# Kernel tuning notes

Measured on AMD Instinct MI355X. Metric: run time of the kernel, lower is better.

Reference implementation:

```python
import jax, jax.numpy as jnp
import numpy as np

DECAY = 0.99
EPS = 1e-05
BETA = 0.25
N_CODES = 1024
CODE_DIM = 128


def setup_inputs() -> dict:
    key = jax.random.key(0)
    k1, k2, k3, k4 = jax.random.split(key, 4)
    z_e = jax.random.normal(k1, (32, CODE_DIM, 32, 32), dtype=jnp.float32)
    embed = jax.random.normal(k2, (N_CODES, CODE_DIM), dtype=jnp.float32)
    cluster_size = jax.random.uniform(k3, (N_CODES,), dtype=jnp.float32) * 10.0
    embed_avg = jax.random.normal(k4, (N_CODES, CODE_DIM), dtype=jnp.float32)
    return {"z_e": z_e, "embed": embed, "cluster_size": cluster_size, "embed_avg": embed_avg}


def reference(z_e, embed, cluster_size, embed_avg):
    B, C, H, W = z_e.shape
    n_codes = embed.shape[0]
    # (B,C,H,W) -> (B*H*W, C)
    flat = jnp.transpose(z_e, (0, 2, 3, 1)).reshape(-1, C).astype(jnp.float32)
    e = embed.astype(jnp.float32)
    d = (flat ** 2).sum(1, keepdims=True) - 2.0 * flat @ e.T + (e ** 2).sum(1)
    idx = jnp.argmin(d, axis=1)
    z_q = embed[idx].reshape(B, H, W, C)
    z_q = jnp.transpose(z_q, (0, 3, 1, 2))  # (B,C,H,W)

    # ---- EMA codebook update (training branch, no-grad in torch) ----
    counts = jax.ops.segment_sum(jnp.ones_like(idx, dtype=jnp.float32), idx,
                                 num_segments=n_codes)
    new_cluster_size = cluster_size * DECAY + (1.0 - DECAY) * counts
    embed_sum = jax.ops.segment_sum(flat, idx, num_segments=n_codes)  # == (flat.T @ one_hot).T
    new_embed_avg = embed_avg * DECAY + (1.0 - DECAY) * embed_sum
    n = new_cluster_size.sum()
    denom = n + n_codes * EPS
    cs = (new_cluster_size + EPS) / denom * n
    cs_safe = jnp.maximum(cs, EPS)[:, None]
    embed_normalized = new_embed_avg / cs_safe
    embed_normalized = jnp.nan_to_num(embed_normalized, nan=0.0, posinf=1.0, neginf=-1.0)
    new_embed = jnp.clip(embed_normalized, -2.0, 2.0)

    # straight-through estimator
    z_q_st = z_e + jax.lax.stop_gradient(z_q - z_e)
    diff = jax.lax.stop_gradient(z_q_st).astype(jnp.float32) - z_e.astype(jnp.float32)
    loss = BETA * jnp.mean(diff ** 2)

    return (z_q_st, loss, idx.reshape(B, H, W), z_q, z_e,
            new_embed, new_cluster_size, new_embed_avg)
```

## Files before the change

### kernel.cpp

```cpp
#include <hip/hip_runtime.h>

#define DECAY 0.99f
#define ONE_MINUS_DECAY 0.01f
#define EPSF 1e-5f
#define BETA 0.25f

constexpr int M_ = 32768;
constexpr int N_ = 1024;
constexpr int K_ = 128;

typedef _Float16 f16;
typedef f16 f16x8 __attribute__((ext_vector_type(8)));
typedef float f32x4 __attribute__((ext_vector_type(4)));

#define GLOAD_LDS(g, l) __builtin_amdgcn_global_load_lds( \
    (const __attribute__((address_space(1))) void*)(g),   \
    (__attribute__((address_space(3))) void*)(l), 16, 0, 0)

#define PINS(p) { unsigned _t2 = m1 > (p) ? m1 : (p); m1 = m1 < (p) ? m1 : (p); \
                  unsigned _t3 = m2 > _t2 ? m2 : _t2;  m2 = m2 < _t2 ? m2 : _t2; \
                  m3 = m3 < _t3 ? m3 : _t3; }

constexpr size_t WS_FLAT   = 0;
constexpr size_t WS_XH     = WS_FLAT   + (size_t)M_ * K_ * 4;
constexpr size_t WS_EH     = WS_XH     + (size_t)M_ * K_ * 2;
constexpr size_t WS_NL     = WS_EH     + (size_t)N_ * K_ * 2;
constexpr size_t WS_PPK    = WS_NL     + (size_t)N_ * 4;
constexpr size_t WS_IDX    = WS_PPK    + (size_t)4 * M_ * 16;
constexpr size_t WS_COUNTS = WS_IDX    + (size_t)M_ * 4;
constexpr size_t WS_CUR    = WS_COUNTS + (size_t)N_ * 4;
constexpr size_t WS_ESUM   = WS_CUR    + (size_t)N_ * 4;
constexpr size_t WS_OFFS   = WS_ESUM   + (size_t)N_ * K_ * 4;
constexpr size_t WS_ROWS   = WS_OFFS   + (size_t)N_ * 4;
constexpr size_t WS_LPART  = WS_ROWS   + (size_t)M_ * 4;
constexpr size_t WS_NSUM   = WS_LPART  + (size_t)4096 * 8;

constexpr size_t O_ZQST = 0;
constexpr size_t O_LOSS = O_ZQST + (size_t)M_ * K_;
constexpr size_t O_IDX  = O_LOSS + 1;
constexpr size_t O_ZQ   = O_IDX  + (size_t)M_;
constexpr size_t O_ZE   = O_ZQ   + (size_t)M_ * K_;
constexpr size_t O_EMB  = O_ZE   + (size_t)M_ * K_;
constexpr size_t O_NCS  = O_EMB  + (size_t)N_ * K_;
constexpr size_t O_NEA  = O_NCS  + (size_t)N_;

__global__ void transpose_kernel(const float* __restrict__ ze,
                                 const float* __restrict__ embed,
                                 float* __restrict__ flat,
                                 f16* __restrict__ xh,
                                 float* __restrict__ out_ze,
                                 f16* __restrict__ eh, float* __restrict__ nl,
                                 uint4* __restrict__ zero8k) {
    __shared__ float tile[128][33];
    __shared__ float ered[2];
    const int j = blockIdx.x;
    const int t = threadIdx.x;
    if (t < 128) {
        float a = embed[(size_t)j * K_ + t];
        eh[(size_t)j * K_ + t] = (f16)(-2.f * a);
        float s = a * a;
        #pragma unroll
        for (int off = 32; off; off >>= 1) s += __shfl_down(s, off);
        if ((t & 63) == 0) ered[t >> 6] = s;
    }
    if (j < 2) zero8k[j * 256 + t] = make_uint4(0u, 0u, 0u, 0u);

    int b = j >> 5, h = j & 31;
    const size_t base = (size_t)b * 131072 + (size_t)h * 32;
    #pragma unroll
    for (int i = 0; i < 4; ++i) {
        int q = i * 256 + t;
        int c = q >> 3, w4 = (q & 7) * 4;
        float4 v = *(const float4*)(ze + base + (size_t)c * 1024 + w4);
        tile[c][w4 + 0] = v.x; tile[c][w4 + 1] = v.y;
        tile[c][w4 + 2] = v.z; tile[c][w4 + 3] = v.w;
        *(float4*)(out_ze + base + (size_t)c * 1024 + w4) = v;
    }
    __syncthreads();
    if (t == 0) nl[j] = ered[0] + ered[1];
    const int r0 = b * 1024 + h * 32;
    #pragma unroll
    for (int i = 0; i < 2; ++i) {
        int w = (t >> 4) + i * 16;
        int c0 = (t & 15) * 8;
        int r = r0 + w;
        float vv[8];
        #pragma unroll
        for (int q = 0; q < 8; ++q) vv[q] = tile[c0 + q][w];
        *(float4*)(flat + (size_t)r * K_ + c0)     = make_float4(vv[0], vv[1], vv[2], vv[3]);
        *(float4*)(flat + (size_t)r * K_ + c0 + 4) = make_float4(vv[4], vv[5], vv[6], vv[7]);
        f16x8 hv;
        #pragma unroll
        for (int q = 0; q < 8; ++q) hv[q] = (f16)vv[q];
        size_t xa = (size_t)r * K_ + ((((c0 >> 3) ^ (r & 15)) << 3));
        *(f16x8*)(xh + xa) = hv;
    }
}

__global__ __launch_bounds__(256, 4)
void nn_kernel(const f16* __restrict__ xh_g,
               const f16* __restrict__ eh, const float* __restrict__ nl,
               uint4* __restrict__ p_pk) {
    __shared__ __align__(16) f16 xbh[64 * 128];
    __shared__ uint4 pm[4][64];
    const int t = threadIdx.x;
    const int wave = t >> 6, lane = t & 63;
    const int crow = lane & 15, g = lane >> 4;
    const int c0 = blockIdx.y * 256 + wave * 64;

    f16x8 efh[4][4];
    #pragma unroll
    for (int m = 0; m < 4; ++m)
        #pragma unroll
        for (int kt = 0; kt < 4; ++kt)
            efh[m][kt] = *(const f16x8*)(eh + (size_t)(c0 + m * 16 + crow) * K_ + kt * 32 + g * 8);
    f32x4 nlinit[4];
    #pragma unroll
    for (int m = 0; m < 4; ++m) {
        f32x4 v = *(const f32x4*)(nl + c0 + m * 16 + g * 4);
        nlinit[m] = v + 1024.f;
    }
    const unsigned cbase = (unsigned)(c0 + g * 4);

    auto stage = [&](int bt) {
        const size_t tb = (size_t)(blockIdx.x * 4 + bt) * 8192;
        #pragma unroll
        for (int i = 0; i < 4; ++i) {
            int q = wave * 4 + i;
            GLOAD_LDS(xh_g + tb + q * 512 + lane * 8, &xbh[q * 512]);
        }
    };

    stage(0);
    __syncthreads();
    for (int bt = 0; bt < 4; ++bt) {
        const int R0 = (blockIdx.x * 4 + bt) * 64;
        #pragma unroll
        for (int st = 0; st < 4; ++st) {
            f32x4 acc[4];
            #pragma unroll
            for (int m = 0; m < 4; ++m) acc[m] = nlinit[m];
            #pragma unroll
            for (int kt = 0; kt < 4; ++kt) {
                int off = (st * 16 + crow) * 128 + ((((kt << 2) + g) ^ crow) << 3);
                f16x8 bh = *(const f16x8*)&xbh[off];
                #pragma unroll
                for (int m = 0; m < 4; ++m)
                    acc[m] = __builtin_amdgcn_mfma_f32_16x16x32_f16(efh[m][kt], bh, acc[m], 0, 0, 0);
            }
            unsigned m1 = ~0u, m2 = ~0u, m3 = ~0u;
            #pragma unroll
            for (int m = 0; m < 4; ++m)
                #pragma unroll
                for (int q = 0; q < 4; ++q) {
                    unsigned u = (unsigned)(acc[m][q] * 1024.f);
                    unsigned p = (u << 10) + cbase + (unsigned)(m * 16 + q);
                    PINS(p);
                }
            #pragma unroll
            for (int d = 16; d <= 32; d <<= 1) {
                unsigned o1 = (unsigned)__shfl_xor((int)m1, d);
                unsigned o2 = (unsigned)__shfl_xor((int)m2, d);
                unsigned o3 = (unsigned)__shfl_xor((int)m3, d);
                PINS(o1); PINS(o2); PINS(o3);
            }
            if (lane < 16) pm[wave][st * 16 + crow] = make_uint4(m1, m2, m3, 0u);
        }
        __syncthreads();
        if (bt < 3) stage(bt + 1);
        if (lane < 16) {
            int row = wave * 16 + lane;
            uint4 a = pm[0][row];
            unsigned m1 = a.x, m2 = a.y, m3 = a.z;
            #pragma unroll
            for (int w = 1; w < 4; ++w) {
                uint4 b = pm[w][row];
                PINS(b.x); PINS(b.y); PINS(b.z);
            }
            p_pk[(size_t)blockIdx.y * M_ + R0 + row] = make_uint4(m1, m2, m3, 0u);
        }
        __syncthreads();
    }
}

__global__ void reduce_refine_kernel(const uint4* __restrict__ p_pk,
                                     const float* __restrict__ flat,
                                     const float* __restrict__ embed,
                                     const float* __restrict__ nl,
                                     int* __restrict__ idxws, float* __restrict__ out_idx,
                                     int* __restrict__ counts) {
    int r = blockIdx.x * 256 + threadIdx.x;
    uint4 a = p_pk[r];
    unsigned m1 = a.x, m2 = a.y, m3 = a.z;
    #pragma unroll
    for (int y = 1; y < 4; ++y) {
        uint4 b = p_pk[(size_t)y * M_ + r];
        PINS(b.x); PINS(b.y); PINS(b.z);
    }
    int i1 = (int)(m1 & 1023u);
    if ((m2 >> 10) - (m1 >> 10) <= 512u) {
        int i2 = (int)(m2 & 1023u), i3 = (int)(m3 & 1023u);
        const float* x  = flat  + (size_t)r * K_;
        const float* e1 = embed + (size_t)i1 * K_;
        const float* e2 = embed + (size_t)i2 * K_;
        const float* e3 = embed + (size_t)i3 * K_;
        float d1 = 0.f, d2 = 0.f, d3 = 0.f;
        for (int k = 0; k < K_; ++k) {
            float xv = x[k];
            d1 = fmaf(xv, e1[k], d1);
            d2 = fmaf(xv, e2[k], d2);
            d3 = fmaf(xv, e3[k], d3);
        }
        float s1 = fmaf(-2.f, d1, nl[i1]);
        float s2 = fmaf(-2.f, d2, nl[i2]);
        float s3 = fmaf(-2.f, d3, nl[i3]);
        float bs = s1; int bi = i1;
        if (s2 < bs || (s2 == bs && i2 < bi)) { bs = s2; bi = i2; }
        if (s3 < bs || (s3 == bs && i3 < bi)) { bs = s3; bi = i3; }
        i1 = bi;
    }
    idxws[r] = i1;
    out_idx[r] = (float)i1;
    atomicAdd(counts + i1, 1);
}

__global__ void gather_kernel(const float* __restrict__ embed,
                              const int* __restrict__ idxws,
                              float* __restrict__ out_st, float* __restrict__ out_zq) {
    int q = blockIdx.x * 256 + threadIdx.x;
    int o0 = q * 4;
    int rbase = (o0 >> 17) * 1024 + (o0 & 1023);
    int c = (o0 >> 10) & 127;
    int4 jj = *(const int4*)(idxws + rbase);
    float4 zq = make_float4(embed[(size_t)jj.x * K_ + c], embed[(size_t)jj.y * K_ + c],
                            embed[(size_t)jj.z * K_ + c], embed[(size_t)jj.w * K_ + c]);
    *(float4*)(out_st + o0) = zq;
    *(float4*)(out_zq + o0) = zq;
}

__global__ void ema_a_kernel(const float* __restrict__ cluster_size,
                             const int* __restrict__ counts,
                             float* __restrict__ out_ncs, float* __restrict__ nws,
                             int* __restrict__ offs) {
    int j = threadIdx.x;
    int cnt = counts[j];
    float ncs = cluster_size[j] * DECAY + ONE_MINUS_DECAY * (float)cnt;
    out_ncs[j] = ncs;
    __shared__ float red[1024];
    __shared__ int sc[1024];
    red[j] = ncs;
    sc[j] = cnt;
    __syncthreads();
    for (int d = 1; d < 1024; d <<= 1) {
        int v = (j >= d) ? sc[j - d] : 0;
        __syncthreads();
        sc[j] += v;
        __syncthreads();
    }
    offs[j] = sc[j] - cnt;
    for (int st = 512; st; st >>= 1) {
        if (j < st) red[j] += red[j + st];
        __syncthreads();
    }
    if (j == 0) nws[0] = red[0];
}

__global__ void bucket_kernel(const int* __restrict__ idxws, const int* __restrict__ offs,
                              int* __restrict__ cur, int* __restrict__ rows,
                              float4* __restrict__ esum_z) {
    __shared__ int lcnt[N_];
    __shared__ int lbase[N_];
    int t = threadIdx.x;
    esum_z[blockIdx.x * 256 + t] = make_float4(0.f, 0.f, 0.f, 0.f);
    #pragma unroll
    for (int i = 0; i < 4; ++i) lcnt[i * 256 + t] = 0;
    __syncthreads();
    int r = blockIdx.x * 256 + t;
    int j = idxws[r];
    atomicAdd(&lcnt[j], 1);
    __syncthreads();
    #pragma unroll
    for (int i = 0; i < 4; ++i) {
        int c = i * 256 + t;
        int n = lcnt[c];
        lbase[c] = n ? atomicAdd(cur + c, n) : 0;
        lcnt[c] = 0;
    }
    __syncthreads();
    int p = atomicAdd(&lcnt[j], 1) + lbase[j];
    rows[offs[j] + p] = r;
}

__global__ void chunksum_kernel(const float* __restrict__ flat,
                                const float* __restrict__ embed,
                                const int* __restrict__ rows,
                                const int* __restrict__ idxws,
                                float* __restrict__ esum,
                                double* __restrict__ lpart) {
    __shared__ int srid[64];
    __shared__ int scd[65];
    __shared__ double lred[128];
    int k = threadIdx.x;
    int b = blockIdx.x;
    if (k < 64) {
        int r = rows[b * 64 + k];
        srid[k] = r;
        scd[k] = idxws[r];
    }
    if (k == 64) scd[64] = -1;
    __syncthreads();
    float acc = 0.f;
    double lacc = 0.0;
    #pragma unroll 1
    for (int i0 = 0; i0 < 64; i0 += 8) {
        float v[8], ev[8];
        #pragma unroll
        for (int i = 0; i < 8; ++i)
            v[i] = flat[(size_t)srid[i0 + i] * K_ + k];
        #pragma unroll
        for (int i = 0; i < 8; ++i)
            ev[i] = embed[(size_t)scd[i0 + i] * K_ + k];
        #pragma unroll
        for (int i = 0; i < 8; ++i) {
            acc += v[i];
            float diff = ev[i] - v[i];
            lacc = fmaf((double)diff, (double)diff, lacc);
            int p = i0 + i;
            if (scd[p + 1] != scd[p]) {
                atomicAdd(esum + (size_t)scd[p] * K_ + k, acc);
                acc = 0.f;
            }
        }
    }
    lred[k] = lacc;
    __syncthreads();
    for (int s = 64; s; s >>= 1) {
        if (k < s) lred[k] += lred[k + s];
        __syncthreads();
    }
    if (k == 0) lpart[b] = lred[0];
}

__global__ void ema_b_kernel(const float* __restrict__ embed_avg,
                             const float* __restrict__ esum,
                             const float* __restrict__ out_ncs,
                             const float* __restrict__ nws,
                             const double* __restrict__ lpart,
                             float* __restrict__ out_nea, float* __restrict__ out_emb,
                             float* __restrict__ out_loss) {
    int o = blockIdx.x * 256 + threadIdx.x;
    int j = o >> 7;
    float navg = embed_avg[o] * DECAY + ONE_MINUS_DECAY * esum[o];
    out_nea[o] = navg;
    float n = nws[0];
    float denom = n + 1024.0f * EPSF;
    float cs = (out_ncs[j] + EPSF) / denom * n;
    float cs_safe = fmaxf(cs, EPSF);
    float v = navg / cs_safe;
    if (v != v) v = 0.f;
    v = fminf(fmaxf(v, -2.f), 2.f);
    out_emb[o] = v;
    if (blockIdx.x == 0) {
        __shared__ double red[256];
        int t = threadIdx.x;
        red[t] = lpart[t] + lpart[t + 256];
        __syncthreads();
        for (int s = 128; s; s >>= 1) {
            if (t < s) red[t] += red[t + s];
            __syncthreads();
        }
        if (t == 0) out_loss[0] = (float)((double)BETA * (red[0] / 4194304.0));
    }
}

extern "C" void kernel_launch(void* const* d_in, const int* in_sizes, int n_in,
                              void* d_out, int out_size, void* d_ws, size_t ws_size,
                              hipStream_t stream) {
    const float* z_e          = (const float*)d_in[0];
    const float* embed        = (const float*)d_in[1];
    const float* cluster_size = (const float*)d_in[2];
    const float* embed_avg    = (const float*)d_in[3];
    float* out = (float*)d_out;
    char*  ws  = (char*)d_ws;

    float*  flat   = (float*)(ws + WS_FLAT);
    f16*    xhp    = (f16*)  (ws + WS_XH);
    f16*    ehp    = (f16*)  (ws + WS_EH);
    float*  nlp    = (float*)(ws + WS_NL);
    uint4*  p_pk   = (uint4*)(ws + WS_PPK);
    int*    idxws  = (int*)  (ws + WS_IDX);
    int*    counts = (int*)  (ws + WS_COUNTS);
    int*    cur    = (int*)  (ws + WS_CUR);
    float*  esum   = (float*)(ws + WS_ESUM);
    int*    offs   = (int*)  (ws + WS_OFFS);
    int*    rows   = (int*)  (ws + WS_ROWS);
    double* lpart  = (double*)(ws + WS_LPART);
    float*  nws    = (float*)(ws + WS_NSUM);

    transpose_kernel<<<1024, 256, 0, stream>>>(z_e, embed, flat, xhp, out + O_ZE,
                                               ehp, nlp, (uint4*)(ws + WS_COUNTS));
    nn_kernel<<<dim3(128, 4), 256, 0, stream>>>(xhp, ehp, nlp, p_pk);
    reduce_refine_kernel<<<M_ / 256, 256, 0, stream>>>(p_pk, flat, embed, nlp,
                                                       idxws, out + O_IDX, counts);
    gather_kernel<<<4096, 256, 0, stream>>>(embed, idxws, out + O_ZQST, out + O_ZQ);
    ema_a_kernel<<<1, 1024, 0, stream>>>(cluster_size, counts, out + O_NCS, nws, offs);
    bucket_kernel<<<M_ / 256, 256, 0, stream>>>(idxws, offs, cur, rows,
                                                (float4*)(ws + WS_ESUM));
    chunksum_kernel<<<M_ / 64, K_, 0, stream>>>(flat, embed, rows, idxws, esum, lpart);
    ema_b_kernel<<<(N_ * K_) / 256, 256, 0, stream>>>(embed_avg, esum, out + O_NCS, nws,
                                                      lpart, out + O_NEA, out + O_EMB,
                                                      out + O_LOSS);
}
```

Baseline: 91.87 us.

## Split nn_kernel into one row tile per block and fuse EMA-A into reduce

The nearest-neighbour kernel now gives each block a single 64-row tile, so the grid grows from 128x4 to 512x4 blocks. This drops the per-block loop over four tiles and its staged prefetch, trading in-block overlap for more blocks in flight. Separately, the single-block ema_a kernel is removed. Its work (new cluster sizes, prefix-sum offsets, total) now runs in the last block of reduce_refine_kernel, found with a done counter and threadfence, which saves a launch and the serial 1024-thread scan. The done counter is zeroed in the transpose kernel.

```diff
diff --git a/kernel.cpp b/kernel.cpp
--- a/kernel.cpp
+++ b/kernel.cpp
@@ -29,7 +29,8 @@
 constexpr size_t WS_IDX    = WS_PPK    + (size_t)4 * M_ * 16;
 constexpr size_t WS_COUNTS = WS_IDX    + (size_t)M_ * 4;
 constexpr size_t WS_CUR    = WS_COUNTS + (size_t)N_ * 4;
-constexpr size_t WS_ESUM   = WS_CUR    + (size_t)N_ * 4;
+constexpr size_t WS_DONE   = WS_CUR    + (size_t)N_ * 4;
+constexpr size_t WS_ESUM   = WS_DONE   + 16;
 constexpr size_t WS_OFFS   = WS_ESUM   + (size_t)N_ * K_ * 4;
 constexpr size_t WS_ROWS   = WS_OFFS   + (size_t)N_ * 4;
 constexpr size_t WS_LPART  = WS_ROWS   + (size_t)M_ * 4;
@@ -64,6 +65,7 @@
         if ((t & 63) == 0) ered[t >> 6] = s;
     }
     if (j < 2) zero8k[j * 256 + t] = make_uint4(0u, 0u, 0u, 0u);
+    if (j == 2 && t == 0) zero8k[512] = make_uint4(0u, 0u, 0u, 0u);
 
     int b = j >> 5, h = j & 31;
     const size_t base = (size_t)b * 131072 + (size_t)h * 32;
@@ -107,6 +109,16 @@
     const int wave = t >> 6, lane = t & 63;
     const int crow = lane & 15, g = lane >> 4;
     const int c0 = blockIdx.y * 256 + wave * 64;
+    const int R0 = blockIdx.x * 64;
+
+    {
+        const size_t tb = (size_t)blockIdx.x * 8192;
+        #pragma unroll
+        for (int i = 0; i < 4; ++i) {
+            int q = wave * 4 + i;
+            GLOAD_LDS(xh_g + tb + q * 512 + lane * 8, &xbh[q * 512]);
+        }
+    }
 
     f16x8 efh[4][4];
     #pragma unroll
@@ -122,64 +134,49 @@
     }
     const unsigned cbase = (unsigned)(c0 + g * 4);
 
-    auto stage = [&](int bt) {
-        const size_t tb = (size_t)(blockIdx.x * 4 + bt) * 8192;
-        #pragma unroll
-        for (int i = 0; i < 4; ++i) {
-            int q = wave * 4 + i;
-            GLOAD_LDS(xh_g + tb + q * 512 + lane * 8, &xbh[q * 512]);
-        }
-    };
-
-    stage(0);
-    __syncthreads();
-    for (int bt = 0; bt < 4; ++bt) {
-        const int R0 = (blockIdx.x * 4 + bt) * 64;
-        #pragma unroll
-        for (int st = 0; st < 4; ++st) {
-            f32x4 acc[4];
-            #pragma unroll
-            for (int m = 0; m < 4; ++m) acc[m] = nlinit[m];
-            #pragma unroll
-            for (int kt = 0; kt < 4; ++kt) {
-                int off = (st * 16 + crow) * 128 + ((((kt << 2) + g) ^ crow) << 3);
-                f16x8 bh = *(const f16x8*)&xbh[off];
-                #pragma unroll
-                for (int m = 0; m < 4; ++m)
-                    acc[m] = __builtin_amdgcn_mfma_f32_16x16x32_f16(efh[m][kt], bh, acc[m], 0, 0, 0);
-            }
-            unsigned m1 = ~0u, m2 = ~0u, m3 = ~0u;
+    __syncthreads();
+    #pragma unroll
+    for (int st = 0; st < 4; ++st) {
+        f32x4 acc[4];
+        #pragma unroll
+        for (int m = 0; m < 4; ++m) acc[m] = nlinit[m];
+        #pragma unroll
+        for (int kt = 0; kt < 4; ++kt) {
+            int off = (st * 16 + crow) * 128 + ((((kt << 2) + g) ^ crow) << 3);
+            f16x8 bh = *(const f16x8*)&xbh[off];
             #pragma unroll
             for (int m = 0; m < 4; ++m)
-                #pragma unroll
-                for (int q = 0; q < 4; ++q) {
-                    unsigned u = (unsigned)(acc[m][q] * 1024.f);
-                    unsigned p = (u << 10) + cbase + (unsigned)(m * 16 + q);
-                    PINS(p);
-                }
+                acc[m] = __builtin_amdgcn_mfma_f32_16x16x32_f16(efh[m][kt], bh, acc[m], 0, 0, 0);
+        }
+        unsigned m1 = ~0u, m2 = ~0u, m3 = ~0u;
+        #pragma unroll
+        for (int m = 0; m < 4; ++m)
             #pragma unroll
-            for (int d = 16; d <= 32; d <<= 1) {
-                unsigned o1 = (unsigned)__shfl_xor((int)m1, d);
-                unsigned o2 = (unsigned)__shfl_xor((int)m2, d);
-                unsigned o3 = (unsigned)__shfl_xor((int)m3, d);
-                PINS(o1); PINS(o2); PINS(o3);
+            for (int q = 0; q < 4; ++q) {
+                unsigned u = (unsigned)(acc[m][q] * 1024.f);
+                unsigned p = (u << 10) + cbase + (unsigned)(m * 16 + q);
+                PINS(p);
             }
-            if (lane < 16) pm[wave][st * 16 + crow] = make_uint4(m1, m2, m3, 0u);
-        }
-        __syncthreads();
-        if (bt < 3) stage(bt + 1);
-        if (lane < 16) {
-            int row = wave * 16 + lane;
-            uint4 a = pm[0][row];
-            unsigned m1 = a.x, m2 = a.y, m3 = a.z;
-            #pragma unroll
-            for (int w = 1; w < 4; ++w) {
-                uint4 b = pm[w][row];
-                PINS(b.x); PINS(b.y); PINS(b.z);
-            }
-            p_pk[(size_t)blockIdx.y * M_ + R0 + row] = make_uint4(m1, m2, m3, 0u);
-        }
-        __syncthreads();
+        #pragma unroll
+        for (int d = 16; d <= 32; d <<= 1) {
+            unsigned o1 = (unsigned)__shfl_xor((int)m1, d);
+            unsigned o2 = (unsigned)__shfl_xor((int)m2, d);
+            unsigned o3 = (unsigned)__shfl_xor((int)m3, d);
+            PINS(o1); PINS(o2); PINS(o3);
+        }
+        if (lane < 16) pm[wave][st * 16 + crow] = make_uint4(m1, m2, m3, 0u);
+    }
+    __syncthreads();
+    if (lane < 16) {
+        int row = wave * 16 + lane;
+        uint4 a = pm[0][row];
+        unsigned m1 = a.x, m2 = a.y, m3 = a.z;
+        #pragma unroll
+        for (int w = 1; w < 4; ++w) {
+            uint4 b = pm[w][row];
+            PINS(b.x); PINS(b.y); PINS(b.z);
+        }
+        p_pk[(size_t)blockIdx.y * M_ + R0 + row] = make_uint4(m1, m2, m3, 0u);
     }
 }
 
@@ -187,8 +184,12 @@
                                      const float* __restrict__ flat,
                                      const float* __restrict__ embed,
                                      const float* __restrict__ nl,
+                                     const float* __restrict__ cluster_size,
                                      int* __restrict__ idxws, float* __restrict__ out_idx,
-                                     int* __restrict__ counts) {
+                                     int* __restrict__ counts,
+                                     unsigned* __restrict__ done,
+                                     float* __restrict__ out_ncs, float* __restrict__ nws,
+                                     int* __restrict__ offs) {
     int r = blockIdx.x * 256 + threadIdx.x;
     uint4 a = p_pk[r];
     unsigned m1 = a.x, m2 = a.y, m3 = a.z;
@@ -222,6 +223,42 @@
     idxws[r] = i1;
     out_idx[r] = (float)i1;
     atomicAdd(counts + i1, 1);
+
+    __shared__ unsigned isLast;
+    __threadfence();
+    if (threadIdx.x == 0) isLast = (atomicAdd(done, 1u) == gridDim.x - 1) ? 1u : 0u;
+    __syncthreads();
+    if (isLast) {
+        const int t = threadIdx.x;
+        __shared__ int sc[256];
+        __shared__ float sf[256];
+        int c4[4], pre[4];
+        float nsum = 0.f;
+        #pragma unroll
+        for (int i = 0; i < 4; ++i) {
+            int j = t * 4 + i;
+            c4[i] = atomicAdd(counts + j, 0);
+            float ncs = cluster_size[j] * DECAY + ONE_MINUS_DECAY * (float)c4[i];
+            out_ncs[j] = ncs;
+            nsum += ncs;
+        }
+        pre[0] = 0; pre[1] = c4[0]; pre[2] = pre[1] + c4[1]; pre[3] = pre[2] + c4[2];
+        int csum = pre[3] + c4[3];
+        sc[t] = csum;
+        sf[t] = nsum;
+        __syncthreads();
+        for (int d = 1; d < 256; d <<= 1) {
+            int v = (t >= d) ? sc[t - d] : 0;
+            float f = (t >= d) ? sf[t - d] : 0.f;
+            __syncthreads();
+            sc[t] += v; sf[t] += f;
+            __syncthreads();
+        }
+        int base = sc[t] - csum;
+        #pragma unroll
+        for (int i = 0; i < 4; ++i) offs[t * 4 + i] = base + pre[i];
+        if (t == 255) nws[0] = sf[255];
+    }
 }
 
 __global__ void gather_kernel(const float* __restrict__ embed,
@@ -236,33 +273,6 @@
                             embed[(size_t)jj.z * K_ + c], embed[(size_t)jj.w * K_ + c]);
     *(float4*)(out_st + o0) = zq;
     *(float4*)(out_zq + o0) = zq;
-}
-
-__global__ void ema_a_kernel(const float* __restrict__ cluster_size,
-                             const int* __restrict__ counts,
-                             float* __restrict__ out_ncs, float* __restrict__ nws,
-                             int* __restrict__ offs) {
-    int j = threadIdx.x;
-    int cnt = counts[j];
-    float ncs = cluster_size[j] * DECAY + ONE_MINUS_DECAY * (float)cnt;
-    out_ncs[j] = ncs;
-    __shared__ float red[1024];
-    __shared__ int sc[1024];
-    red[j] = ncs;
-    sc[j] = cnt;
-    __syncthreads();
-    for (int d = 1; d < 1024; d <<= 1) {
-        int v = (j >= d) ? sc[j - d] : 0;
-        __syncthreads();
-        sc[j] += v;
-        __syncthreads();
-    }
-    offs[j] = sc[j] - cnt;
-    for (int st = 512; st; st >>= 1) {
-        if (j < st) red[j] += red[j + st];
-        __syncthreads();
-    }
-    if (j == 0) nws[0] = red[0];
 }
 
 __global__ void bucket_kernel(const int* __restrict__ idxws, const int* __restrict__ offs,
@@ -383,27 +393,28 @@
     float* out = (float*)d_out;
     char*  ws  = (char*)d_ws;
 
-    float*  flat   = (float*)(ws + WS_FLAT);
-    f16*    xhp    = (f16*)  (ws + WS_XH);
-    f16*    ehp    = (f16*)  (ws + WS_EH);
-    float*  nlp    = (float*)(ws + WS_NL);
-    uint4*  p_pk   = (uint4*)(ws + WS_PPK);
-    int*    idxws  = (int*)  (ws + WS_IDX);
-    int*    counts = (int*)  (ws + WS_COUNTS);
-    int*    cur    = (int*)  (ws + WS_CUR);
-    float*  esum   = (float*)(ws + WS_ESUM);
-    int*    offs   = (int*)  (ws + WS_OFFS);
-    int*    rows   = (int*)  (ws + WS_ROWS);
-    double* lpart  = (double*)(ws + WS_LPART);
-    float*  nws    = (float*)(ws + WS_NSUM);
+    float*    flat   = (float*)(ws + WS_FLAT);
+    f16*      xhp    = (f16*)  (ws + WS_XH);
+    f16*      ehp    = (f16*)  (ws + WS_EH);
+    float*    nlp    = (float*)(ws + WS_NL);
+    uint4*    p_pk   = (uint4*)(ws + WS_PPK);
+    int*      idxws  = (int*)  (ws + WS_IDX);
+    int*      counts = (int*)  (ws + WS_COUNTS);
+    int*      cur    = (int*)  (ws + WS_CUR);
+    unsigned* done   = (unsigned*)(ws + WS_DONE);
+    float*    esum   = (float*)(ws + WS_ESUM);
+    int*      offs   = (int*)  (ws + WS_OFFS);
+    int*      rows   = (int*)  (ws + WS_ROWS);
+    double*   lpart  = (double*)(ws + WS_LPART);
+    float*    nws    = (float*)(ws + WS_NSUM);
 
     transpose_kernel<<<1024, 256, 0, stream>>>(z_e, embed, flat, xhp, out + O_ZE,
                                                ehp, nlp, (uint4*)(ws + WS_COUNTS));
-    nn_kernel<<<dim3(128, 4), 256, 0, stream>>>(xhp, ehp, nlp, p_pk);
+    nn_kernel<<<dim3(512, 4), 256, 0, stream>>>(xhp, ehp, nlp, p_pk);
     reduce_refine_kernel<<<M_ / 256, 256, 0, stream>>>(p_pk, flat, embed, nlp,
-                                                       idxws, out + O_IDX, counts);
+                                                       cluster_size, idxws, out + O_IDX,
+                                                       counts, done, out + O_NCS, nws, offs);
     gather_kernel<<<4096, 256, 0, stream>>>(embed, idxws, out + O_ZQST, out + O_ZQ);
-    ema_a_kernel<<<1, 1024, 0, stream>>>(cluster_size, counts, out + O_NCS, nws, offs);
     bucket_kernel<<<M_ / 256, 256, 0, stream>>>(idxws, offs, cur, rows,
                                                 (float4*)(ws + WS_ESUM));
     chunksum_kernel<<<M_ / 64, K_, 0, stream>>>(flat, embed, rows, idxws, esum, lpart);
```

Result: slower. 95.29 us (+3.7%).
